# Kernel optimization log

Hardware: AMD Instinct MI355X
Metric: run time of the kernel (lower is better)

The kernel has to match this reference:

```python
import jax, jax.numpy as jnp
import numpy as np

LN_EPS = 1e-5


def setup_inputs() -> dict:
    key = jax.random.key(0)
    k1, k2, k3, k4, k5 = jax.random.split(key, 5)
    V, D_REAL, D_HID, D_MODEL = 32000, 768, 512, 4096
    B, S = 4, 2048
    return {
        "real": jax.random.normal(k1, (V, D_REAL), dtype=jnp.float32),
        "llama_embed": jax.random.normal(k2, (V, D_MODEL), dtype=jnp.float32),
        "w1": jax.random.normal(k3, (D_HID, D_REAL), dtype=jnp.float32),  # trans_1.weight
        "w2": jax.random.normal(k4, (D_MODEL, D_HID), dtype=jnp.float32),  # trans_2.weight
        "ln_w": jnp.ones((D_HID,), dtype=jnp.float32),
        "ln_b": jnp.zeros((D_HID,), dtype=jnp.float32),
        "input_ids": jax.random.randint(k5, (B, S), 0, V, dtype=jnp.int64),
    }


def _layernorm(x, w, b):
    mu = jnp.mean(x, axis=-1, keepdims=True)
    var = jnp.mean(jnp.square(x - mu), axis=-1, keepdims=True)
    return (x - mu) * jax.lax.rsqrt(var + LN_EPS) * w + b


def reference(real, llama_embed, w1, w2, ln_w, ln_b, input_ids):
    # trans_2(ELU(LayerNorm(trans_1(real)))) over the FULL table, as in the original
    h = jnp.einsum("vd,hd->vh", real, w1)            # [V, 512]
    h = jax.nn.elu(_layernorm(h, ln_w, ln_b))        # [V, 512]
    transfered = jnp.einsum("vh,mh->vm", h, w2)      # [V, 4096]
    # gather rows per token and add frozen llama embeddings
    return transfered[input_ids] + llama_embed[input_ids]  # [B, S, 4096]
```

## Files before the change

kernel.cpp:

```cpp
#include <hip/hip_runtime.h>
#include <hip/hip_bf16.h>
#include <math.h>

#define TOKENS 8192
#define D_REAL 768
#define D_HID  512
#define D_MODEL 4096

typedef __attribute__((ext_vector_type(8))) short bf16x8;
typedef __attribute__((ext_vector_type(4))) float f32x4;

__device__ inline unsigned short f2bf(float f) {
    union { float f; unsigned u; } v; v.f = f;
    unsigned r = v.u + 0x7FFFu + ((v.u >> 16) & 1u);
    return (unsigned short)(r >> 16);
}
__device__ inline float bf2f(unsigned short h) {
    union { unsigned u; float f; } v; v.u = ((unsigned)h) << 16;
    return v.f;
}

__device__ inline void gload_lds16(const void* g, void* lds_wave_base) {
    __builtin_amdgcn_global_load_lds(
        (const __attribute__((address_space(1))) unsigned*)g,
        (__attribute__((address_space(3))) unsigned*)lds_wave_base,
        16, 0, 0);
}

__device__ inline void BAR() {
    asm volatile("" ::: "memory");
    __builtin_amdgcn_s_barrier();
    asm volatile("" ::: "memory");
}

__global__ __launch_bounds__(256)
void gemm1_mfma(const unsigned short* __restrict__ A,
                const unsigned short* __restrict__ B,
                unsigned short* __restrict__ C)
{
    constexpr int K = D_REAL, N = D_HID;
    __shared__ __align__(16) unsigned short As[64 * 32];
    __shared__ __align__(16) unsigned short Bs[128 * 32];

    const int tid = threadIdx.x;
    const int rowBase = blockIdx.x * 64;
    const int colBase = blockIdx.y * 128;

    const int srow = tid >> 2;
    const int scol = (tid & 3) * 8;
    const unsigned short* gA = A + (size_t)(rowBase + srow) * K + scol;
    const unsigned short* gB = B + (size_t)(colBase + srow) * K + scol;
    unsigned short* lA = As + (tid >> 6) * 512;
    unsigned short* lB = Bs + (tid >> 6) * 512;

    const int lane = tid & 63;
    const int wv   = tid >> 6;
    const int wm   = (wv >> 1) * 32;
    const int wn   = (wv & 1) * 64;
    const int frow = lane & 15;
    const int fk   = (lane >> 4) * 8;

    f32x4 acc[2][4];
    #pragma unroll
    for (int i = 0; i < 2; i++)
        #pragma unroll
        for (int j = 0; j < 4; j++) acc[i][j] = (f32x4)0.f;

    for (int k0 = 0; k0 < K; k0 += 32) {
        gload_lds16(gA,                lA);
        gload_lds16(gB,                lB);
        gload_lds16(gB + (size_t)64*K, lB + 2048);
        gA += 32; gB += 32;
        __syncthreads();

        bf16x8 af[2], bg[4];
        #pragma unroll
        for (int i = 0; i < 2; i++)
            af[i] = *reinterpret_cast<const bf16x8*>(&As[(wm + i*16 + frow) * 32 + fk]);
        #pragma unroll
        for (int j = 0; j < 4; j++)
            bg[j] = *reinterpret_cast<const bf16x8*>(&Bs[(wn + j*16 + frow) * 32 + fk]);

        #pragma unroll
        for (int i = 0; i < 2; i++)
            #pragma unroll
            for (int j = 0; j < 4; j++)
                acc[i][j] = __builtin_amdgcn_mfma_f32_16x16x32_bf16(af[i], bg[j], acc[i][j], 0, 0, 0);
        __syncthreads();
    }

    const int orow0 = wm + (lane >> 4) * 4;
    const int ocol0 = wn + frow;
    #pragma unroll
    for (int i = 0; i < 2; i++)
        #pragma unroll
        for (int r = 0; r < 4; r++) {
            unsigned short* dst = C + (size_t)(rowBase + orow0 + i*16 + r) * N + colBase + ocol0;
            #pragma unroll
            for (int j = 0; j < 4; j++)
                dst[j * 16] = f2bf(acc[i][j][r]);
        }
}

__global__ __launch_bounds__(512, 2)
void gemm2_8phase(const unsigned short* __restrict__ A,
                  const unsigned short* __restrict__ B,
                  const int* __restrict__ ids,
                  const float* __restrict__ embed,
                  float* __restrict__ C)
{
    constexpr int K = D_HID, N = D_MODEL, NKT = K / 64;
    __shared__ __align__(16) unsigned short lds[65536];
    __shared__ int sIds[256];
    unsigned short* Alds = lds;
    unsigned short* Blds = lds + 32768;

    const int f   = blockIdx.x;
    const int xcd = f & 7;
    const int idx = f >> 3;
    const int rowBase = (xcd * 4 + (idx & 3)) * 256;
    const int colBase = (idx >> 2) * 256;

    const int tid  = threadIdx.x;
    const int lane = tid & 63;
    const int wv   = tid >> 6;
    const int wr   = wv >> 2;
    const int wc   = wv & 3;
    const int frow = lane & 15;
    const int fq   = lane >> 4;

    if (tid < 256) sIds[tid] = ids[rowBase + tid];

    auto STAGE_HALF = [&](const unsigned short* Mp, unsigned short* Ml,
                          int tileBase, int kt, int h) {
        const int buf = kt & 1;
        #pragma unroll
        for (int u = 0; u < 2; ++u) {
            const int c    = u * 512 + tid;
            const int row  = c >> 3;
            const int slot = (c & 7) ^ (row & 7);
            const unsigned short* g = Mp + (size_t)(tileBase + h * 128 + row) * K
                                         + kt * 64 + slot * 8;
            unsigned short* l = Ml + (buf * 2 + h) * 8192 + (u * 512 + wv * 64) * 8;
            gload_lds16(g, l);
        }
    };
    auto STAGE = [&](int kt_s, int h_s) {
        if (kt_s >= NKT) return;
        if (h_s < 2) STAGE_HALF(A, Alds, rowBase, kt_s, h_s);
        else         STAGE_HALF(B, Blds, colBase, kt_s, h_s - 2);
    };
    auto LDA = [&](int buf, int mf, int kk) -> bf16x8 {
        const int row  = mf * 16 + frow;
        const int slot = (kk * 4 + fq) ^ (row & 7);
        return *reinterpret_cast<const bf16x8*>(
            Alds + (buf * 2 + wr) * 8192 + row * 64 + slot * 8);
    };
    auto LDB = [&](int buf, int nf, int kk) -> bf16x8 {
        const int rb   = wc * 64 + nf * 16 + frow;
        const int row  = rb & 127;
        const int slot = (kk * 4 + fq) ^ (row & 7);
        return *reinterpret_cast<const bf16x8*>(
            Blds + (buf * 2 + (rb >> 7)) * 8192 + row * 64 + slot * 8);
    };

    f32x4 acc[8][4];
    #pragma unroll
    for (int i = 0; i < 8; i++)
        #pragma unroll
        for (int j = 0; j < 4; j++) acc[i][j] = (f32x4)0.f;

    STAGE(0, 0); STAGE(0, 1); STAGE(0, 2); STAGE(0, 3); STAGE(1, 0);
    asm volatile("s_waitcnt vmcnt(2)" ::: "memory");
    __builtin_amdgcn_s_barrier();
    asm volatile("" ::: "memory");

    #pragma unroll
    for (int kt = 0; kt < NKT; ++kt) {
        const int buf = kt & 1;
        bf16x8 bg[4][2];
        #pragma unroll
        for (int p = 0; p < 4; ++p) {
            bf16x8 af[2][2];
            #pragma unroll
            for (int i = 0; i < 2; ++i)
                #pragma unroll
                for (int kk = 0; kk < 2; ++kk)
                    af[i][kk] = LDA(buf, p * 2 + i, kk);
            if (p == 0) {
                #pragma unroll
                for (int nf = 0; nf < 4; ++nf)
                    #pragma unroll
                    for (int kk = 0; kk < 2; ++kk)
                        bg[nf][kk] = LDB(buf, nf, kk);
            }
            if (p < 3) STAGE(kt + 1, p + 1);
            BAR();
            if (p == 3) STAGE(kt + 2, 0);
            __builtin_amdgcn_s_setprio(1);
            #pragma unroll
            for (int i = 0; i < 2; ++i)
                #pragma unroll
                for (int nf = 0; nf < 4; ++nf)
                    #pragma unroll
                    for (int kk = 0; kk < 2; ++kk)
                        acc[p*2+i][nf] = __builtin_amdgcn_mfma_f32_16x16x32_bf16(
                            af[i][kk], bg[nf][kk], acc[p*2+i][nf], 0, 0, 0);
            __builtin_amdgcn_s_setprio(0);
            if (p == 3) {
                if (kt + 2 < NKT)      asm volatile("s_waitcnt vmcnt(2)" ::: "memory");
                else if (kt + 1 < NKT) asm volatile("s_waitcnt vmcnt(0)" ::: "memory");
            }
            BAR();
        }
    }

    const int ocol0 = colBase + wc * 64 + frow;
    #pragma unroll
    for (int mf = 0; mf < 8; ++mf) {
        #pragma unroll
        for (int r = 0; r < 4; ++r) {
            const int lrow = wr * 128 + mf * 16 + fq * 4 + r;
            const float* e = embed + (size_t)sIds[lrow] * N + ocol0;
            float* o = C + (size_t)(rowBase + lrow) * N + ocol0;
            #pragma unroll
            for (int nf = 0; nf < 4; ++nf)
                o[nf * 16] = acc[mf][nf][r] + e[nf * 16];
        }
    }
}

__global__ __launch_bounds__(256)
void convert2_bf16(const float* __restrict__ s1, unsigned short* __restrict__ d1, int n1,
                   const float* __restrict__ s2, unsigned short* __restrict__ d2, int n2)
{
    int i = blockIdx.x * 256 + threadIdx.x;
    const float* src; unsigned short* dst;
    if (i < n1) { src = s1; dst = d1; }
    else {
        i -= n1;
        if (i >= n2) return;
        src = s2; dst = d2;
    }
    const float4 v = reinterpret_cast<const float4*>(src)[i];
    ushort4 o;
    o.x = f2bf(v.x); o.y = f2bf(v.y); o.z = f2bf(v.z); o.w = f2bf(v.w);
    reinterpret_cast<ushort4*>(dst)[i] = o;
}

__global__ __launch_bounds__(192)
void gather_bf16(const float* __restrict__ real, const int* __restrict__ ids,
                 unsigned short* __restrict__ Ag)
{
    const int row = blockIdx.x;
    const int t = threadIdx.x;
    const float4 v = *reinterpret_cast<const float4*>(real + (size_t)ids[row] * D_REAL + t * 4);
    ushort4 o;
    o.x = f2bf(v.x); o.y = f2bf(v.y); o.z = f2bf(v.z); o.w = f2bf(v.w);
    *reinterpret_cast<ushort4*>(Ag + (size_t)row * D_REAL + t * 4) = o;
}

__global__ __launch_bounds__(256)
void ln_elu_bf16(unsigned short* __restrict__ H,
                 const float* __restrict__ ln_w, const float* __restrict__ ln_b)
{
    const int row = blockIdx.x * 4 + (threadIdx.x >> 6);
    const int t = threadIdx.x & 63;
    unsigned short* x = H + (size_t)row * D_HID + t * 8;

    bf16x8 v = *reinterpret_cast<const bf16x8*>(x);
    float fv[8], s = 0.f, ss = 0.f;
    #pragma unroll
    for (int j = 0; j < 8; j++) {
        fv[j] = bf2f((unsigned short)v[j]);
        s += fv[j]; ss += fv[j] * fv[j];
    }
    #pragma unroll
    for (int off = 32; off > 0; off >>= 1) {
        s  += __shfl_down(s, off);
        ss += __shfl_down(ss, off);
    }
    s = __shfl(s, 0); ss = __shfl(ss, 0);
    const float mu = s * (1.f / D_HID);
    const float var = ss * (1.f / D_HID) - mu * mu;
    const float rstd = rsqrtf(var + 1e-5f);

    const float4 w0 = *reinterpret_cast<const float4*>(ln_w + t * 8);
    const float4 w1 = *reinterpret_cast<const float4*>(ln_w + t * 8 + 4);
    const float4 b0 = *reinterpret_cast<const float4*>(ln_b + t * 8);
    const float4 b1 = *reinterpret_cast<const float4*>(ln_b + t * 8 + 4);
    const float wa[8] = { w0.x, w0.y, w0.z, w0.w, w1.x, w1.y, w1.z, w1.w };
    const float ba[8] = { b0.x, b0.y, b0.z, b0.w, b1.x, b1.y, b1.z, b1.w };

    bf16x8 o;
    #pragma unroll
    for (int j = 0; j < 8; j++) {
        float y = (fv[j] - mu) * rstd * wa[j] + ba[j];
        y = y > 0.f ? y : expm1f(y);
        o[j] = (short)f2bf(y);
    }
    *reinterpret_cast<bf16x8*>(x) = o;
}

extern "C" void kernel_launch(void* const* d_in, const int* in_sizes, int n_in,
                              void* d_out, int out_size, void* d_ws, size_t ws_size,
                              hipStream_t stream)
{
    const float* real  = (const float*)d_in[0];
    const float* embed = (const float*)d_in[1];
    const float* w1    = (const float*)d_in[2];
    const float* w2    = (const float*)d_in[3];
    const float* ln_w  = (const float*)d_in[4];
    const float* ln_b  = (const float*)d_in[5];
    const int*   ids   = (const int*)d_in[6];
    float* out = (float*)d_out;

    unsigned short* Hb  = (unsigned short*)d_ws;
    unsigned short* w1b = Hb  + (size_t)TOKENS * D_HID;
    unsigned short* w2b = w1b + (size_t)D_HID * D_REAL;
    unsigned short* Ag  = (unsigned short*)d_out;

    const int n1 = D_HID * D_REAL / 4, n2 = D_MODEL * D_HID / 4;
    convert2_bf16<<<(n1 + n2 + 255) / 256, 256, 0, stream>>>(w1, w1b, n1, w2, w2b, n2);
    gather_bf16<<<TOKENS, 192, 0, stream>>>(real, ids, Ag);

    dim3 g1(TOKENS / 64, D_HID / 128);
    gemm1_mfma<<<g1, 256, 0, stream>>>(Ag, w1b, Hb);

    ln_elu_bf16<<<TOKENS / 4, 256, 0, stream>>>(Hb, ln_w, ln_b);

    gemm2_8phase<<<512, 512, 0, stream>>>(Hb, w2b, ids, embed, out);
}
```

Baseline: 124.3 us.

## Fuse token gather into GEMM1 and shrink GEMM2 tiles to 128x128

The separate gather+convert kernel is removed. GEMM1 now reads the fp32 rows of `real` for each token id directly, converts them to bf16 in registers and stores them to LDS, which saves one launch and a round trip through global memory. GEMM2 moves from 256x256 tiles with 512 blocks to 128x128 tiles with 2048 blocks and half the LDS, aiming for higher occupancy and better load balance. The costs are lower data reuse per tile and a synchronous global-to-register path for the A operand in GEMM1.

```diff
diff --git a/kernel.cpp b/kernel.cpp
--- a/kernel.cpp
+++ b/kernel.cpp
@@ -18,6 +18,14 @@
 __device__ inline float bf2f(unsigned short h) {
     union { unsigned u; float f; } v; v.u = ((unsigned)h) << 16;
     return v.f;
+}
+__device__ inline bf16x8 cvt8(float4 a, float4 b) {
+    bf16x8 r;
+    r[0] = (short)f2bf(a.x); r[1] = (short)f2bf(a.y);
+    r[2] = (short)f2bf(a.z); r[3] = (short)f2bf(a.w);
+    r[4] = (short)f2bf(b.x); r[5] = (short)f2bf(b.y);
+    r[6] = (short)f2bf(b.z); r[7] = (short)f2bf(b.w);
+    return r;
 }
 
 __device__ inline void gload_lds16(const void* g, void* lds_wave_base) {
@@ -34,23 +42,26 @@
 }
 
 __global__ __launch_bounds__(256)
-void gemm1_mfma(const unsigned short* __restrict__ A,
+void gemm1_mfma(const float* __restrict__ real, const int* __restrict__ ids,
                 const unsigned short* __restrict__ B,
                 unsigned short* __restrict__ C)
 {
     constexpr int K = D_REAL, N = D_HID;
     __shared__ __align__(16) unsigned short As[64 * 32];
     __shared__ __align__(16) unsigned short Bs[128 * 32];
+    __shared__ int sIds[64];
 
     const int tid = threadIdx.x;
     const int rowBase = blockIdx.x * 64;
     const int colBase = blockIdx.y * 128;
 
+    if (tid < 64) sIds[tid] = ids[rowBase + tid];
+    __syncthreads();
+
     const int srow = tid >> 2;
     const int scol = (tid & 3) * 8;
-    const unsigned short* gA = A + (size_t)(rowBase + srow) * K + scol;
+    const float* gA = real + (size_t)sIds[srow] * K + scol;
     const unsigned short* gB = B + (size_t)(colBase + srow) * K + scol;
-    unsigned short* lA = As + (tid >> 6) * 512;
     unsigned short* lB = Bs + (tid >> 6) * 512;
 
     const int lane = tid & 63;
@@ -67,10 +78,11 @@
         for (int j = 0; j < 4; j++) acc[i][j] = (f32x4)0.f;
 
     for (int k0 = 0; k0 < K; k0 += 32) {
-        gload_lds16(gA,                lA);
-        gload_lds16(gB,                lB);
-        gload_lds16(gB + (size_t)64*K, lB + 2048);
-        gA += 32; gB += 32;
+        gload_lds16(gB + k0,                lB);
+        gload_lds16(gB + k0 + (size_t)64*K, lB + 2048);
+        const float4 a0 = *reinterpret_cast<const float4*>(gA + k0);
+        const float4 a1 = *reinterpret_cast<const float4*>(gA + k0 + 4);
+        *reinterpret_cast<bf16x8*>(&As[srow * 32 + scol]) = cvt8(a0, a1);
         __syncthreads();
 
         bf16x8 af[2], bg[4];
@@ -102,24 +114,24 @@
         }
 }
 
-__global__ __launch_bounds__(512, 2)
-void gemm2_8phase(const unsigned short* __restrict__ A,
-                  const unsigned short* __restrict__ B,
-                  const int* __restrict__ ids,
-                  const float* __restrict__ embed,
-                  float* __restrict__ C)
+__global__ __launch_bounds__(512, 4)
+void gemm2_mfma(const unsigned short* __restrict__ A,
+                const unsigned short* __restrict__ B,
+                const int* __restrict__ ids,
+                const float* __restrict__ embed,
+                float* __restrict__ C)
 {
     constexpr int K = D_HID, N = D_MODEL, NKT = K / 64;
-    __shared__ __align__(16) unsigned short lds[65536];
-    __shared__ int sIds[256];
-    unsigned short* Alds = lds;
-    unsigned short* Blds = lds + 32768;
+    __shared__ __align__(16) unsigned short lds2[32768];
+    __shared__ int sIds[128];
+    unsigned short* Alds = lds2;
+    unsigned short* Blds = lds2 + 16384;
 
     const int f   = blockIdx.x;
     const int xcd = f & 7;
     const int idx = f >> 3;
-    const int rowBase = (xcd * 4 + (idx & 3)) * 256;
-    const int colBase = (idx >> 2) * 256;
+    const int rowBase = (xcd * 8 + (idx & 7)) * 128;
+    const int colBase = (idx >> 3) * 128;
 
     const int tid  = threadIdx.x;
     const int lane = tid & 63;
@@ -129,48 +141,42 @@
     const int frow = lane & 15;
     const int fq   = lane >> 4;
 
-    if (tid < 256) sIds[tid] = ids[rowBase + tid];
-
-    auto STAGE_HALF = [&](const unsigned short* Mp, unsigned short* Ml,
-                          int tileBase, int kt, int h) {
-        const int buf = kt & 1;
+    if (tid < 128) sIds[tid] = ids[rowBase + tid];
+
+    auto STAGE = [&](const unsigned short* Mp, unsigned short* Ml,
+                     int tileBase, int kt) {
+        if (kt >= NKT) return;
+        unsigned short* Mb = Ml + (kt & 1) * 8192;
         #pragma unroll
         for (int u = 0; u < 2; ++u) {
             const int c    = u * 512 + tid;
             const int row  = c >> 3;
             const int slot = (c & 7) ^ (row & 7);
-            const unsigned short* g = Mp + (size_t)(tileBase + h * 128 + row) * K
+            const unsigned short* g = Mp + (size_t)(tileBase + row) * K
                                          + kt * 64 + slot * 8;
-            unsigned short* l = Ml + (buf * 2 + h) * 8192 + (u * 512 + wv * 64) * 8;
-            gload_lds16(g, l);
+            gload_lds16(g, Mb + (u * 512 + wv * 64) * 8);
         }
     };
-    auto STAGE = [&](int kt_s, int h_s) {
-        if (kt_s >= NKT) return;
-        if (h_s < 2) STAGE_HALF(A, Alds, rowBase, kt_s, h_s);
-        else         STAGE_HALF(B, Blds, colBase, kt_s, h_s - 2);
-    };
     auto LDA = [&](int buf, int mf, int kk) -> bf16x8 {
-        const int row  = mf * 16 + frow;
+        const int row  = wr * 64 + mf * 16 + frow;
         const int slot = (kk * 4 + fq) ^ (row & 7);
-        return *reinterpret_cast<const bf16x8*>(
-            Alds + (buf * 2 + wr) * 8192 + row * 64 + slot * 8);
+        return *reinterpret_cast<const bf16x8*>(Alds + buf * 8192 + row * 64 + slot * 8);
     };
     auto LDB = [&](int buf, int nf, int kk) -> bf16x8 {
-        const int rb   = wc * 64 + nf * 16 + frow;
-        const int row  = rb & 127;
+        const int row  = wc * 32 + nf * 16 + frow;
         const int slot = (kk * 4 + fq) ^ (row & 7);
-        return *reinterpret_cast<const bf16x8*>(
-            Blds + (buf * 2 + (rb >> 7)) * 8192 + row * 64 + slot * 8);
+        return *reinterpret_cast<const bf16x8*>(Blds + buf * 8192 + row * 64 + slot * 8);
     };
 
-    f32x4 acc[8][4];
-    #pragma unroll
-    for (int i = 0; i < 8; i++)
-        #pragma unroll
-        for (int j = 0; j < 4; j++) acc[i][j] = (f32x4)0.f;
-
-    STAGE(0, 0); STAGE(0, 1); STAGE(0, 2); STAGE(0, 3); STAGE(1, 0);
+    f32x4 acc[4][2];
+    #pragma unroll
+    for (int i = 0; i < 4; i++)
+        #pragma unroll
+        for (int j = 0; j < 2; j++) acc[i][j] = (f32x4)0.f;
+
+    STAGE(A, Alds, rowBase, 0);
+    STAGE(B, Blds, colBase, 0);
+    STAGE(A, Alds, rowBase, 1);
     asm volatile("s_waitcnt vmcnt(2)" ::: "memory");
     __builtin_amdgcn_s_barrier();
     asm volatile("" ::: "memory");
@@ -178,53 +184,63 @@
     #pragma unroll
     for (int kt = 0; kt < NKT; ++kt) {
         const int buf = kt & 1;
-        bf16x8 bg[4][2];
-        #pragma unroll
-        for (int p = 0; p < 4; ++p) {
-            bf16x8 af[2][2];
-            #pragma unroll
-            for (int i = 0; i < 2; ++i)
+        bf16x8 af0[2][2], bg[2][2];
+        #pragma unroll
+        for (int i = 0; i < 2; ++i)
+            #pragma unroll
+            for (int kk = 0; kk < 2; ++kk)
+                af0[i][kk] = LDA(buf, i, kk);
+        #pragma unroll
+        for (int nf = 0; nf < 2; ++nf)
+            #pragma unroll
+            for (int kk = 0; kk < 2; ++kk)
+                bg[nf][kk] = LDB(buf, nf, kk);
+        STAGE(B, Blds, colBase, kt + 1);
+        BAR();
+        __builtin_amdgcn_s_setprio(1);
+        #pragma unroll
+        for (int i = 0; i < 2; ++i)
+            #pragma unroll
+            for (int nf = 0; nf < 2; ++nf)
                 #pragma unroll
                 for (int kk = 0; kk < 2; ++kk)
-                    af[i][kk] = LDA(buf, p * 2 + i, kk);
-            if (p == 0) {
+                    acc[i][nf] = __builtin_amdgcn_mfma_f32_16x16x32_bf16(
+                        af0[i][kk], bg[nf][kk], acc[i][nf], 0, 0, 0);
+        __builtin_amdgcn_s_setprio(0);
+        BAR();
+        bf16x8 af1[2][2];
+        #pragma unroll
+        for (int i = 0; i < 2; ++i)
+            #pragma unroll
+            for (int kk = 0; kk < 2; ++kk)
+                af1[i][kk] = LDA(buf, 2 + i, kk);
+        BAR();
+        STAGE(A, Alds, rowBase, kt + 2);
+        __builtin_amdgcn_s_setprio(1);
+        #pragma unroll
+        for (int i = 0; i < 2; ++i)
+            #pragma unroll
+            for (int nf = 0; nf < 2; ++nf)
                 #pragma unroll
-                for (int nf = 0; nf < 4; ++nf)
-                    #pragma unroll
-                    for (int kk = 0; kk < 2; ++kk)
-                        bg[nf][kk] = LDB(buf, nf, kk);
-            }
-            if (p < 3) STAGE(kt + 1, p + 1);
-            BAR();
-            if (p == 3) STAGE(kt + 2, 0);
-            __builtin_amdgcn_s_setprio(1);
-            #pragma unroll
-            for (int i = 0; i < 2; ++i)
-                #pragma unroll
-                for (int nf = 0; nf < 4; ++nf)
-                    #pragma unroll
-                    for (int kk = 0; kk < 2; ++kk)
-                        acc[p*2+i][nf] = __builtin_amdgcn_mfma_f32_16x16x32_bf16(
-                            af[i][kk], bg[nf][kk], acc[p*2+i][nf], 0, 0, 0);
-            __builtin_amdgcn_s_setprio(0);
-            if (p == 3) {
-                if (kt + 2 < NKT)      asm volatile("s_waitcnt vmcnt(2)" ::: "memory");
-                else if (kt + 1 < NKT) asm volatile("s_waitcnt vmcnt(0)" ::: "memory");
-            }
-            BAR();
-        }
-    }
-
-    const int ocol0 = colBase + wc * 64 + frow;
-    #pragma unroll
-    for (int mf = 0; mf < 8; ++mf) {
+                for (int kk = 0; kk < 2; ++kk)
+                    acc[2 + i][nf] = __builtin_amdgcn_mfma_f32_16x16x32_bf16(
+                        af1[i][kk], bg[nf][kk], acc[2 + i][nf], 0, 0, 0);
+        __builtin_amdgcn_s_setprio(0);
+        if (kt + 2 < NKT)      asm volatile("s_waitcnt vmcnt(2)" ::: "memory");
+        else if (kt + 1 < NKT) asm volatile("s_waitcnt vmcnt(0)" ::: "memory");
+        BAR();
+    }
+
+    const int ocol0 = colBase + wc * 32 + frow;
+    #pragma unroll
+    for (int mf = 0; mf < 4; ++mf) {
         #pragma unroll
         for (int r = 0; r < 4; ++r) {
-            const int lrow = wr * 128 + mf * 16 + fq * 4 + r;
+            const int lrow = wr * 64 + mf * 16 + fq * 4 + r;
             const float* e = embed + (size_t)sIds[lrow] * N + ocol0;
             float* o = C + (size_t)(rowBase + lrow) * N + ocol0;
             #pragma unroll
-            for (int nf = 0; nf < 4; ++nf)
+            for (int nf = 0; nf < 2; ++nf)
                 o[nf * 16] = acc[mf][nf][r] + e[nf * 16];
         }
     }
@@ -246,18 +262,6 @@
     ushort4 o;
     o.x = f2bf(v.x); o.y = f2bf(v.y); o.z = f2bf(v.z); o.w = f2bf(v.w);
     reinterpret_cast<ushort4*>(dst)[i] = o;
-}
-
-__global__ __launch_bounds__(192)
-void gather_bf16(const float* __restrict__ real, const int* __restrict__ ids,
-                 unsigned short* __restrict__ Ag)
-{
-    const int row = blockIdx.x;
-    const int t = threadIdx.x;
-    const float4 v = *reinterpret_cast<const float4*>(real + (size_t)ids[row] * D_REAL + t * 4);
-    ushort4 o;
-    o.x = f2bf(v.x); o.y = f2bf(v.y); o.z = f2bf(v.z); o.w = f2bf(v.w);
-    *reinterpret_cast<ushort4*>(Ag + (size_t)row * D_REAL + t * 4) = o;
 }
 
 __global__ __launch_bounds__(256)
@@ -318,16 +322,14 @@
     unsigned short* Hb  = (unsigned short*)d_ws;
     unsigned short* w1b = Hb  + (size_t)TOKENS * D_HID;
     unsigned short* w2b = w1b + (size_t)D_HID * D_REAL;
-    unsigned short* Ag  = (unsigned short*)d_out;
 
     const int n1 = D_HID * D_REAL / 4, n2 = D_MODEL * D_HID / 4;
     convert2_bf16<<<(n1 + n2 + 255) / 256, 256, 0, stream>>>(w1, w1b, n1, w2, w2b, n2);
-    gather_bf16<<<TOKENS, 192, 0, stream>>>(real, ids, Ag);
 
     dim3 g1(TOKENS / 64, D_HID / 128);
-    gemm1_mfma<<<g1, 256, 0, stream>>>(Ag, w1b, Hb);
+    gemm1_mfma<<<g1, 256, 0, stream>>>(real, ids, w1b, Hb);
 
     ln_elu_bf16<<<TOKENS / 4, 256, 0, stream>>>(Hb, ln_w, ln_b);
 
-    gemm2_8phase<<<512, 512, 0, stream>>>(Hb, w2b, ids, embed, out);
-}
+    gemm2_mfma<<<2048, 512, 0, stream>>>(Hb, w2b, ids, embed, out);
+}
```

After: 126.1 us. About the same (+1.4%).
